# Kernel tuning notes

Hardware: AMD Instinct MI355X
Metric: run time of the kernel (lower is better)

## Reference

```python
import jax, jax.numpy as jnp
import numpy as np
from jax import lax

GAIN = 16.0           # encoder_gains[0]
TEMP = 0.3            # soft_round_temperature
MASK = 9              # mask_size
PAD = 4               # (MASK - 1) // 2
# dim_arm = 16 causal taps inside the 9x9 mask (all indices < center index 40)
CTX_IDX = [12, 13, 14, 20, 21, 22, 23, 24, 28, 29, 30, 31, 32, 33, 38, 39]
CTX_OFF = [(i // MASK, i % MASK) for i in CTX_IDX]
IMG_H, IMG_W = 1024, 1536
N_GRIDS = 7
SIZES = [(int(np.ceil(IMG_H / 2 ** i)), int(np.ceil(IMG_W / 2 ** i))) for i in range(N_GRIDS)]
N_TOTAL = sum(h * w for h, w in SIZES)  # 2097024


def _softround(x, t):
    fl = jnp.floor(x)
    return fl + 0.5 * jnp.tanh((x - fl - 0.5) / t) / jnp.tanh(0.5 / t) + 0.5


def _forward(latents, noise_u, arm_w1, arm_b1, arm_w2, arm_b2, arm_wo, arm_bo,
             ups_k, pre_k, syn_w1, syn_b1, syn_w2, syn_b2):
    # --- quantize latents: softround(softround(x*g) + kumaraswamy noise), a=1 -> uniform-0.5 ---
    flat = jnp.concatenate([l.reshape(-1) for l in latents]) * GAIN
    flat_q = _softround(_softround(flat, TEMP) + (noise_u - 0.5), TEMP)
    dec, cnt = [], 0
    for h, w in SIZES:
        dec.append(flat_q[cnt:cnt + h * w].reshape(1, 1, h, w))
        cnt += h * w
    # --- _get_neighbor: masked causal context gather (16 taps of the 9x9 mask) ---
    ctxs = []
    for l in dec:
        h, w = l.shape[2], l.shape[3]
        xp = jnp.pad(l[0, 0], PAD)  # zero pad, matches F.pad constant 0
        ctxs.append(jnp.stack([xp[dy:dy + h, dx:dx + w] for dy, dx in CTX_OFF], axis=-1).reshape(-1, len(CTX_OFF)))
    ctx = jnp.concatenate(ctxs, axis=0)  # [N, 16]
    # --- ARM MLP: residual hidden layers, final linear to (mu, log_scale) ---
    h1 = jax.nn.relu(ctx @ arm_w1.T + arm_b1 + ctx)
    h2 = jax.nn.relu(h1 @ arm_w2.T + arm_b2 + h1)
    raw = h2 @ arm_wo.T + arm_bo
    mu, log_s = raw[:, 0], raw[:, 1]
    scale = jnp.exp(-0.5 * jnp.clip(log_s, -13.8155, 13.8155))
    def lcdf(x):
        return 0.5 - 0.5 * jnp.sign(x - mu) * jnp.expm1(-jnp.abs(x - mu) / scale)
    proba = jnp.maximum(lcdf(flat_q + 0.5) - lcdf(flat_q - 0.5), 2.0 ** -16)
    rate = -jnp.log2(proba)
    # --- upsampling: coarse-to-fine, depthwise separable convT x2 + preconcat filter ---
    x = dec[-1]
    for step, i in enumerate(range(N_GRIDS - 1, 0, -1)):
        c = x.shape[1]
        kern = jnp.broadcast_to(jnp.outer(ups_k[step], ups_k[step])[None, None], (c, 1, 8, 8))
        x = lax.conv_general_dilated(x, kern, (1, 1), ((4, 4), (4, 4)), lhs_dilation=(2, 2),
                                     dimension_numbers=('NCHW', 'OIHW', 'NCHW'), feature_group_count=c)
        ht, wt = SIZES[i - 1]
        x = x[:, :, :ht, :wt]
        pk2 = jnp.outer(pre_k[step], pre_k[step])[None, None]  # (1,1,7,7)
        t = lax.conv_general_dilated(dec[i - 1], pk2, (1, 1), ((3, 3), (3, 3)),
                                     dimension_numbers=('NCHW', 'OIHW', 'NCHW'))
        x = jnp.concatenate([t, x], axis=1)
    # --- synthesis: 1x1 conv 7->48 relu, 48->6, split mean / log_scale ---
    hid = jax.nn.relu(jnp.einsum('bchw,oc->bohw', x, syn_w1) + syn_b1[None, :, None, None])
    out = jnp.einsum('bchw,oc->bohw', hid, syn_w2) + syn_b2[None, :, None, None]
    pixel_mean, pixel_log_scale = out[:, :3], out[:, 3:]
    # F.interpolate to img_size is identity here (already full resolution)
    decoded = jnp.clip(pixel_mean, 0.0, 1.0)
    return pixel_mean, pixel_log_scale, decoded, rate


def setup_inputs():
    key = jax.random.key(0)
    ks = jax.random.split(key, 16)
    d = {}
    for i, (h, w) in enumerate(SIZES):
        d['latent%d' % i] = jax.random.uniform(ks[i], (1, 1, h, w), jnp.float32, -0.5, 0.5)
    d['noise_u'] = jax.random.uniform(ks[7], (N_TOTAL,), jnp.float32)
    d['arm_w1'] = jax.random.normal(ks[8], (16, 16), jnp.float32) * 0.25
    d['arm_b1'] = jnp.zeros((16,), jnp.float32)
    d['arm_w2'] = jax.random.normal(ks[9], (16, 16), jnp.float32) * 0.25
    d['arm_b2'] = jnp.zeros((16,), jnp.float32)
    d['arm_wo'] = jax.random.normal(ks[10], (2, 16), jnp.float32) * 0.25
    d['arm_bo'] = jnp.zeros((2,), jnp.float32)
    d['ups_k'] = jax.random.normal(ks[11], (6, 8), jnp.float32) * 0.2 + 0.125
    d['pre_k'] = jax.random.normal(ks[12], (6, 7), jnp.float32) * 0.2 + 0.1
    d['syn_w1'] = jax.random.normal(ks[13], (48, 7), jnp.float32) * 0.3
    d['syn_b1'] = jnp.zeros((48,), jnp.float32)
    d['syn_w2'] = jax.random.normal(ks[14], (6, 48), jnp.float32) * 0.1
    d['syn_b2'] = jnp.zeros((6,), jnp.float32)
    return d


def reference(latent0, latent1, latent2, latent3, latent4, latent5, latent6, noise_u,
              arm_w1, arm_b1, arm_w2, arm_b2, arm_wo, arm_bo,
              ups_k, pre_k, syn_w1, syn_b1, syn_w2, syn_b2):
    return _forward([latent0, latent1, latent2, latent3, latent4, latent5, latent6], noise_u,
                    arm_w1, arm_b1, arm_w2, arm_b2, arm_wo, arm_bo,
                    ups_k, pre_k, syn_w1, syn_b1, syn_w2, syn_b2)
```

## Files before the change

kernel.cpp:

```cpp
#include <hip/hip_runtime.h>
#include <math.h>

#define N_TOTAL 2097024
#define HWF (1024 * 1536)

#define OFF0 0
#define OFF1 1572864
#define OFF2 1966080
#define OFF3 2064384
#define OFF4 2088960
#define OFF5 2095104
#define OFF6 2096640

#define OUT_LS   (3 * HWF)
#define OUT_DEC  (6 * HWF)
#define OUT_RATE (9 * HWF)

typedef float f4 __attribute__((ext_vector_type(4), aligned(4)));

__device__ __forceinline__ float softround_f(float x) {
    const float INV_T = 1.0f / 0.3f;
    const float HALF_OVER_TANH = 0.53699381f;
    float fl = floorf(x);
    return fl + tanhf((x - fl - 0.5f) * INV_T) * HALF_OVER_TANH + 0.5f;
}

__global__ void quant_kernel(const float* __restrict__ l0, const float* __restrict__ l1,
                             const float* __restrict__ l2, const float* __restrict__ l3,
                             const float* __restrict__ l4, const float* __restrict__ l5,
                             const float* __restrict__ l6, const float* __restrict__ noise,
                             float* __restrict__ flat_q) {
    int idx = blockIdx.x * blockDim.x + threadIdx.x;
    if (idx >= N_TOTAL) return;
    float v;
    if      (idx < OFF1) v = l0[idx - OFF0];
    else if (idx < OFF2) v = l1[idx - OFF1];
    else if (idx < OFF3) v = l2[idx - OFF2];
    else if (idx < OFF4) v = l3[idx - OFF3];
    else if (idx < OFF5) v = l4[idx - OFF4];
    else if (idx < OFF6) v = l5[idx - OFF5];
    else                 v = l6[idx - OFF6];
    float x = v * 16.0f;
    float s1 = softround_f(x);
    float s2 = softround_f(s1 + noise[idx] - 0.5f);
    flat_q[idx] = s2;
}

template <int H, int W, int OFFT>
__device__ __forceinline__ void arm_body(const float* __restrict__ flat_q, int pos,
                                         const float* __restrict__ w1, const float* __restrict__ b1,
                                         const float* __restrict__ w2, const float* __restrict__ b2,
                                         const float* __restrict__ wo, const float* __restrict__ bo,
                                         float* __restrict__ rate_out) {
    if (pos >= H * W) return;
    unsigned up = (unsigned)pos;
    int y = up / (unsigned)W;
    int x = pos - y * W;
    const float* g = flat_q + OFFT;

    const int DY[16] = {-3,-3,-3,-2,-2,-2,-2,-2,-1,-1,-1,-1,-1,-1, 0, 0};
    const int DX[16] = {-1, 0, 1,-2,-1, 0, 1, 2,-3,-2,-1, 0, 1, 2,-2,-1};
    float ctx[16];
#pragma unroll
    for (int k = 0; k < 16; k++) {
        int yy = y + DY[k], xx = x + DX[k];
        ctx[k] = (yy >= 0 && yy < H && xx >= 0 && xx < W) ? g[yy * W + xx] : 0.0f;
    }

    float h1[16];
#pragma unroll 4
    for (int j = 0; j < 16; j++) {
        float acc = b1[j] + ctx[j];
#pragma unroll
        for (int k = 0; k < 16; k++) acc = fmaf(w1[j * 16 + k], ctx[k], acc);
        h1[j] = fmaxf(acc, 0.0f);
    }
    float h2[16];
#pragma unroll 4
    for (int j = 0; j < 16; j++) {
        float acc = b2[j] + h1[j];
#pragma unroll
        for (int k = 0; k < 16; k++) acc = fmaf(w2[j * 16 + k], h1[k], acc);
        h2[j] = fmaxf(acc, 0.0f);
    }
    float mu = bo[0], ls = bo[1];
#pragma unroll
    for (int k = 0; k < 16; k++) {
        mu = fmaf(wo[k], h2[k], mu);
        ls = fmaf(wo[16 + k], h2[k], ls);
    }
    ls = fminf(fmaxf(ls, -13.8155f), 13.8155f);
    float inv_scale = expf(0.5f * ls);

    float q = g[(size_t)y * W + x];
    float da = (q + 0.5f) - mu;
    float db = (q - 0.5f) - mu;
    float la = 0.5f - 0.5f * copysignf(1.0f, da) * expm1f(-fabsf(da) * inv_scale);
    float lb = 0.5f - 0.5f * copysignf(1.0f, db) * expm1f(-fabsf(db) * inv_scale);
    float proba = fmaxf(la - lb, 1.52587890625e-05f);
    rate_out[OFFT + pos] = -log2f(proba);
}

__global__ __launch_bounds__(256) void arm_all_kernel(
    const float* __restrict__ flat_q,
    const float* __restrict__ w1, const float* __restrict__ b1,
    const float* __restrict__ w2, const float* __restrict__ b2,
    const float* __restrict__ wo, const float* __restrict__ bo,
    float* __restrict__ rate_out) {
    int b = blockIdx.x;
    int t = threadIdx.x;
    if (b < 6144) {
        arm_body<1024, 1536, OFF0>(flat_q, b * 256 + t, w1, b1, w2, b2, wo, bo, rate_out);
    } else if (b < 7680) {
        arm_body<512, 768, OFF1>(flat_q, (b - 6144) * 256 + t, w1, b1, w2, b2, wo, bo, rate_out);
    } else if (b < 8064) {
        arm_body<256, 384, OFF2>(flat_q, (b - 7680) * 256 + t, w1, b1, w2, b2, wo, bo, rate_out);
    } else if (b < 8160) {
        arm_body<128, 192, OFF3>(flat_q, (b - 8064) * 256 + t, w1, b1, w2, b2, wo, bo, rate_out);
    } else if (b < 8184) {
        arm_body<64, 96, OFF4>(flat_q, (b - 8160) * 256 + t, w1, b1, w2, b2, wo, bo, rate_out);
    } else if (b < 8190) {
        arm_body<32, 48, OFF5>(flat_q, (b - 8184) * 256 + t, w1, b1, w2, b2, wo, bo, rate_out);
    } else {
        arm_body<16, 24, OFF6>(flat_q, (b - 8190) * 256 + t, w1, b1, w2, b2, wo, bo, rate_out);
    }
}

__device__ __forceinline__ void up_quad(const float* __restrict__ in, int H, int W,
                                        int i, int j, const float* K, float o[4]) {
    float w[5][5];
    bool interior = (i >= 2 && i <= H - 3 && j >= 2 && j <= W - 3);
    if (interior) {
        const float* p = in + (i - 2) * W + (j - 2);
#pragma unroll
        for (int r = 0; r < 5; r++) {
            f4 a = *(const f4*)p;
            w[r][0] = a.x; w[r][1] = a.y; w[r][2] = a.z; w[r][3] = a.w;
            w[r][4] = p[4];
            p += W;
        }
    } else {
#pragma unroll
        for (int r = 0; r < 5; r++)
#pragma unroll
            for (int e = 0; e < 5; e++) {
                int yy = i - 2 + r, xx = j - 2 + e;
                w[r][e] = (yy >= 0 && yy < H && xx >= 0 && xx < W) ? in[yy * W + xx] : 0.0f;
            }
    }
    float h0[5], h1[5];
#pragma unroll
    for (int r = 0; r < 5; r++) {
        h0[r] = K[0]*w[r][0] + K[2]*w[r][1] + K[4]*w[r][2] + K[6]*w[r][3];
        h1[r] = K[1]*w[r][1] + K[3]*w[r][2] + K[5]*w[r][3] + K[7]*w[r][4];
    }
    o[0] = K[0]*h0[0] + K[2]*h0[1] + K[4]*h0[2] + K[6]*h0[3];
    o[1] = K[0]*h1[0] + K[2]*h1[1] + K[4]*h1[2] + K[6]*h1[3];
    o[2] = K[1]*h0[1] + K[3]*h0[2] + K[5]*h0[3] + K[7]*h0[4];
    o[3] = K[1]*h1[1] + K[3]*h1[2] + K[5]*h1[3] + K[7]*h1[4];
}

__device__ __forceinline__ void conv7_quad(const float* __restrict__ dec, int H, int W,
                                           int i, int j, const float* k, float o[4]) {
    int Y = 2 * i, X = 2 * j;
    float g0[8], g1[8];
    bool interior = (Y - 3 >= 0 && Y + 4 <= H - 1 && X - 3 >= 0 && X + 4 <= W - 1);
    if (interior) {
        const float* p = dec + (Y - 3) * W + (X - 3);
#pragma unroll
        for (int r = 0; r < 8; r++) {
            f4 a = *(const f4*)p;
            f4 b = *(const f4*)(p + 4);
            g0[r] = k[0]*a.x + k[1]*a.y + k[2]*a.z + k[3]*a.w + k[4]*b.x + k[5]*b.y + k[6]*b.z;
            g1[r] = k[0]*a.y + k[1]*a.z + k[2]*a.w + k[3]*b.x + k[4]*b.y + k[5]*b.z + k[6]*b.w;
            p += W;
        }
    } else {
#pragma unroll
        for (int r = 0; r < 8; r++) {
            float wv[8];
#pragma unroll
            for (int q = 0; q < 8; q++) {
                int yy = Y - 3 + r, xx = X - 3 + q;
                wv[q] = (yy >= 0 && yy < H && xx >= 0 && xx < W) ? dec[yy * W + xx] : 0.0f;
            }
            g0[r] = k[0]*wv[0] + k[1]*wv[1] + k[2]*wv[2] + k[3]*wv[3] + k[4]*wv[4] + k[5]*wv[5] + k[6]*wv[6];
            g1[r] = k[0]*wv[1] + k[1]*wv[2] + k[2]*wv[3] + k[3]*wv[4] + k[4]*wv[5] + k[5]*wv[6] + k[6]*wv[7];
        }
    }
    o[0] = k[0]*g0[0] + k[1]*g0[1] + k[2]*g0[2] + k[3]*g0[3] + k[4]*g0[4] + k[5]*g0[5] + k[6]*g0[6];
    o[1] = k[0]*g1[0] + k[1]*g1[1] + k[2]*g1[2] + k[3]*g1[3] + k[4]*g1[4] + k[5]*g1[5] + k[6]*g1[6];
    o[2] = k[0]*g0[1] + k[1]*g0[2] + k[2]*g0[3] + k[3]*g0[4] + k[4]*g0[5] + k[5]*g0[6] + k[6]*g0[7];
    o[3] = k[0]*g1[1] + k[1]*g1[2] + k[2]*g1[3] + k[3]*g1[4] + k[4]*g1[5] + k[5]*g1[6] + k[6]*g1[7];
}

__global__ void pyramid_quad_kernel(const float* __restrict__ xin, int hin, int win_,
                                    const float* __restrict__ dec,
                                    const float* __restrict__ upsk, const float* __restrict__ prek,
                                    float* __restrict__ xout, int hout, int wout) {
    int qw = wout >> 1, qh = hout >> 1;
    int j = blockIdx.x * blockDim.x + threadIdx.x;
    int i = blockIdx.y * blockDim.y + threadIdx.y;
    int c = blockIdx.z;
    if (j >= qw || i >= qh) return;
    float o[4];
    if (c == 0) {
        float k[7];
#pragma unroll
        for (int p = 0; p < 7; p++) k[p] = prek[p];
        conv7_quad(dec, hout, wout, i, j, k, o);
    } else {
        float K[8];
#pragma unroll
        for (int p = 0; p < 8; p++) K[p] = upsk[p];
        up_quad(xin + (size_t)(c - 1) * hin * win_, hin, win_, i, j, K, o);
    }
    size_t base = ((size_t)c * hout + 2 * i) * wout + 2 * j;
    *(float2*)(xout + base)        = make_float2(o[0], o[1]);
    *(float2*)(xout + base + wout) = make_float2(o[2], o[3]);
}

__global__ __launch_bounds__(256) void final_kernel(
    const float* __restrict__ up_in,
    const float* __restrict__ dec0,
    const float* __restrict__ upsk, const float* __restrict__ prek,
    const float* __restrict__ w1, const float* __restrict__ b1,
    const float* __restrict__ w2, const float* __restrict__ b2,
    float* __restrict__ out) {
    const int H2_ = 512, W2_ = 768, H1_ = 1024, W1_ = 1536;
    int t = threadIdx.x;
    int j = blockIdx.x * 16 + (t & 15);
    int i = blockIdx.y * 16 + (t >> 4);

    float K[8], kp[7];
#pragma unroll
    for (int p = 0; p < 8; p++) K[p] = upsk[p];
#pragma unroll
    for (int p = 0; p < 7; p++) kp[p] = prek[p];

    float px0[7], px1[7], px2[7], px3[7];
    {
        float o[4];
        conv7_quad(dec0, H1_, W1_, i, j, kp, o);
        px0[0] = o[0]; px1[0] = o[1]; px2[0] = o[2]; px3[0] = o[3];
    }
#pragma unroll
    for (int c = 0; c < 6; c++) {
        float o[4];
        up_quad(up_in + (size_t)c * (H2_ * W2_), H2_, W2_, i, j, K, o);
        px0[c + 1] = o[0]; px1[c + 1] = o[1]; px2[c + 1] = o[2]; px3[c + 1] = o[3];
    }

    float o0[6], o1[6], o2[6], o3[6];
#pragma unroll
    for (int q = 0; q < 6; q++) {
        float bq = b2[q];
        o0[q] = bq; o1[q] = bq; o2[q] = bq; o3[q] = bq;
    }
#pragma unroll 4
    for (int k = 0; k < 48; k++) {
        float bk = b1[k];
        float a0 = bk, a1 = bk, a2 = bk, a3 = bk;
#pragma unroll
        for (int c = 0; c < 7; c++) {
            float wk = w1[k * 7 + c];
            a0 = fmaf(wk, px0[c], a0);
            a1 = fmaf(wk, px1[c], a1);
            a2 = fmaf(wk, px2[c], a2);
            a3 = fmaf(wk, px3[c], a3);
        }
        a0 = fmaxf(a0, 0.0f); a1 = fmaxf(a1, 0.0f); a2 = fmaxf(a2, 0.0f); a3 = fmaxf(a3, 0.0f);
#pragma unroll
        for (int q = 0; q < 6; q++) {
            float wj = w2[q * 48 + k];
            o0[q] = fmaf(wj, a0, o0[q]);
            o1[q] = fmaf(wj, a1, o1[q]);
            o2[q] = fmaf(wj, a2, o2[q]);
            o3[q] = fmaf(wj, a3, o3[q]);
        }
    }

    size_t base = (size_t)(2 * i) * W1_ + 2 * j;
#pragma unroll
    for (int c = 0; c < 3; c++) {
        *(float2*)(out + (size_t)c * HWF + base)       = make_float2(o0[c], o1[c]);
        *(float2*)(out + (size_t)c * HWF + base + W1_) = make_float2(o2[c], o3[c]);
        *(float2*)(out + OUT_LS + (size_t)c * HWF + base)       = make_float2(o0[c + 3], o1[c + 3]);
        *(float2*)(out + OUT_LS + (size_t)c * HWF + base + W1_) = make_float2(o2[c + 3], o3[c + 3]);
        *(float2*)(out + OUT_DEC + (size_t)c * HWF + base) =
            make_float2(fminf(fmaxf(o0[c], 0.0f), 1.0f), fminf(fmaxf(o1[c], 0.0f), 1.0f));
        *(float2*)(out + OUT_DEC + (size_t)c * HWF + base + W1_) =
            make_float2(fminf(fmaxf(o2[c], 0.0f), 1.0f), fminf(fmaxf(o3[c], 0.0f), 1.0f));
    }
}

extern "C" void kernel_launch(void* const* d_in, const int* in_sizes, int n_in,
                              void* d_out, int out_size, void* d_ws, size_t ws_size,
                              hipStream_t stream) {
    const float* lat[7];
    for (int i = 0; i < 7; i++) lat[i] = (const float*)d_in[i];
    const float* noise  = (const float*)d_in[7];
    const float* arm_w1 = (const float*)d_in[8];
    const float* arm_b1 = (const float*)d_in[9];
    const float* arm_w2 = (const float*)d_in[10];
    const float* arm_b2 = (const float*)d_in[11];
    const float* arm_wo = (const float*)d_in[12];
    const float* arm_bo = (const float*)d_in[13];
    const float* ups_k  = (const float*)d_in[14];
    const float* pre_k  = (const float*)d_in[15];
    const float* syn_w1 = (const float*)d_in[16];
    const float* syn_b1 = (const float*)d_in[17];
    const float* syn_w2 = (const float*)d_in[18];
    const float* syn_b2 = (const float*)d_in[19];
    float* out = (float*)d_out;

    float* flat_q = (float*)d_ws;
    float* bufA   = flat_q + N_TOTAL;
    float* bufB   = bufA + 6 * 512 * 768;

    static const int SH[7]  = {1024, 512, 256, 128, 64, 32, 16};
    static const int SW[7]  = {1536, 768, 384, 192, 96, 48, 24};
    static const int OFF[7] = {OFF0, OFF1, OFF2, OFF3, OFF4, OFF5, OFF6};

    quant_kernel<<<(N_TOTAL + 255) / 256, 256, 0, stream>>>(
        lat[0], lat[1], lat[2], lat[3], lat[4], lat[5], lat[6], noise, flat_q);

    arm_all_kernel<<<8192, 256, 0, stream>>>(flat_q, arm_w1, arm_b1, arm_w2, arm_b2,
                                             arm_wo, arm_bo, out + OUT_RATE);

    const float* xin = flat_q + OFF6;
    float* bufs[2] = {bufA, bufB};
    for (int s = 0; s < 5; s++) {
        int i    = 6 - s;
        int hin  = SH[i], win_ = SW[i];
        int hout = SH[i - 1], wout = SW[i - 1];
        int cin  = s + 1;
        float* xout = bufs[s & 1];
        dim3 blk(16, 16);
        dim3 grd((wout / 2 + 15) / 16, (hout / 2 + 15) / 16, cin + 1);
        pyramid_quad_kernel<<<grd, blk, 0, stream>>>(xin, hin, win_,
                                                     flat_q + OFF[i - 1],
                                                     ups_k + s * 8, pre_k + s * 7,
                                                     xout, hout, wout);
        xin = xout;
    }

    dim3 fgrd(768 / 16, 512 / 16);
    final_kernel<<<fgrd, 256, 0, stream>>>(bufA, flat_q,
                                           ups_k + 5 * 8, pre_k + 5 * 7,
                                           syn_w1, syn_b1, syn_w2, syn_b2, out);
}
```

Baseline: 149.6 us.

## Use packed fp16 dot2 for synthesis MLP and fast tanh in softround

```diff
diff --git a/kernel.cpp b/kernel.cpp
--- a/kernel.cpp
+++ b/kernel.cpp
@@ -17,12 +17,52 @@
 #define OUT_RATE (9 * HWF)
 
 typedef float f4 __attribute__((ext_vector_type(4), aligned(4)));
+typedef _Float16 h2 __attribute__((ext_vector_type(2)));
+typedef __fp16 fp16v2 __attribute__((ext_vector_type(2)));
+
+__device__ __forceinline__ h2 as_h2(unsigned u) {
+    union { unsigned u; h2 h; } x; x.u = u; return x.h;
+}
+__device__ __forceinline__ h2 pkrtz(float a, float b) {
+    union { fp16v2 f; h2 h; } x;
+    x.f = __builtin_amdgcn_cvt_pkrtz(a, b);
+    return x.h;
+}
+__device__ __forceinline__ float dot2f(h2 a, h2 b, float c) {
+#if __has_builtin(__builtin_amdgcn_fdot2)
+    return __builtin_amdgcn_fdot2(a, b, c, false);
+#else
+    return fmaf((float)a[0], (float)b[0], fmaf((float)a[1], (float)b[1], c));
+#endif
+}
 
 __device__ __forceinline__ float softround_f(float x) {
     const float INV_T = 1.0f / 0.3f;
     const float HALF_OVER_TANH = 0.53699381f;
     float fl = floorf(x);
-    return fl + tanhf((x - fl - 0.5f) * INV_T) * HALF_OVER_TANH + 0.5f;
+    float z = (x - fl - 0.5f) * INV_T;
+    float e = __expf(2.0f * z);
+    float th = 1.0f - 2.0f * __builtin_amdgcn_rcpf(e + 1.0f);
+    return fl + th * HALF_OVER_TANH + 0.5f;
+}
+
+__global__ void pack_weights_kernel(const float* __restrict__ w1, const float* __restrict__ b1,
+                                    const float* __restrict__ w2, unsigned* __restrict__ wp) {
+    int t = threadIdx.x;
+    if (t < 192) {
+        int k = t >> 2, p = t & 3;
+        float x = w1[k * 7 + 2 * p];
+        float y = (p < 3) ? w1[k * 7 + 2 * p + 1] : b1[k];
+        union { h2 h; unsigned u; } c;
+        c.h = (h2){(_Float16)x, (_Float16)y};
+        wp[t] = c.u;
+    } else if (t < 336) {
+        int r = t - 192;
+        int o = r / 24, kk = r - o * 24;
+        union { h2 h; unsigned u; } c;
+        c.h = (h2){(_Float16)w2[o * 48 + 2 * kk], (_Float16)w2[o * 48 + 2 * kk + 1]};
+        wp[t] = c.u;
+    }
 }
 
 __global__ void quant_kernel(const float* __restrict__ l0, const float* __restrict__ l1,
@@ -75,19 +115,19 @@
         for (int k = 0; k < 16; k++) acc = fmaf(w1[j * 16 + k], ctx[k], acc);
         h1[j] = fmaxf(acc, 0.0f);
     }
-    float h2[16];
+    float h2v[16];
 #pragma unroll 4
     for (int j = 0; j < 16; j++) {
         float acc = b2[j] + h1[j];
 #pragma unroll
         for (int k = 0; k < 16; k++) acc = fmaf(w2[j * 16 + k], h1[k], acc);
-        h2[j] = fmaxf(acc, 0.0f);
+        h2v[j] = fmaxf(acc, 0.0f);
     }
     float mu = bo[0], ls = bo[1];
 #pragma unroll
     for (int k = 0; k < 16; k++) {
-        mu = fmaf(wo[k], h2[k], mu);
-        ls = fmaf(wo[16 + k], h2[k], ls);
+        mu = fmaf(wo[k], h2v[k], mu);
+        ls = fmaf(wo[16 + k], h2v[k], ls);
     }
     ls = fminf(fmaxf(ls, -13.8155f), 13.8155f);
     float inv_scale = expf(0.5f * ls);
@@ -224,8 +264,8 @@
     const float* __restrict__ up_in,
     const float* __restrict__ dec0,
     const float* __restrict__ upsk, const float* __restrict__ prek,
-    const float* __restrict__ w1, const float* __restrict__ b1,
-    const float* __restrict__ w2, const float* __restrict__ b2,
+    const unsigned* __restrict__ wp,
+    const float* __restrict__ b2,
     float* __restrict__ out) {
     const int H2_ = 512, W2_ = 768, H1_ = 1024, W1_ = 1536;
     int t = threadIdx.x;
@@ -251,46 +291,72 @@
         px0[c + 1] = o[0]; px1[c + 1] = o[1]; px2[c + 1] = o[2]; px3[c + 1] = o[3];
     }
 
-    float o0[6], o1[6], o2[6], o3[6];
-#pragma unroll
-    for (int q = 0; q < 6; q++) {
-        float bq = b2[q];
-        o0[q] = bq; o1[q] = bq; o2[q] = bq; o3[q] = bq;
-    }
+    h2 pp[4][4];
+#pragma unroll
+    for (int c = 0; c < 3; c++) {
+        pp[0][c] = pkrtz(px0[2 * c], px0[2 * c + 1]);
+        pp[1][c] = pkrtz(px1[2 * c], px1[2 * c + 1]);
+        pp[2][c] = pkrtz(px2[2 * c], px2[2 * c + 1]);
+        pp[3][c] = pkrtz(px3[2 * c], px3[2 * c + 1]);
+    }
+    pp[0][3] = pkrtz(px0[6], 1.0f);
+    pp[1][3] = pkrtz(px1[6], 1.0f);
+    pp[2][3] = pkrtz(px2[6], 1.0f);
+    pp[3][3] = pkrtz(px3[6], 1.0f);
+
+    float acc[6][4];
+#pragma unroll
+    for (int o = 0; o < 6; o++) {
+        float b = b2[o];
+#pragma unroll
+        for (int q = 0; q < 4; q++) acc[o][q] = b;
+    }
+    const unsigned* w1p = wp;
+    const unsigned* w2p = wp + 192;
 #pragma unroll 4
-    for (int k = 0; k < 48; k++) {
-        float bk = b1[k];
-        float a0 = bk, a1 = bk, a2 = bk, a3 = bk;
-#pragma unroll
-        for (int c = 0; c < 7; c++) {
-            float wk = w1[k * 7 + c];
-            a0 = fmaf(wk, px0[c], a0);
-            a1 = fmaf(wk, px1[c], a1);
-            a2 = fmaf(wk, px2[c], a2);
-            a3 = fmaf(wk, px3[c], a3);
-        }
-        a0 = fmaxf(a0, 0.0f); a1 = fmaxf(a1, 0.0f); a2 = fmaxf(a2, 0.0f); a3 = fmaxf(a3, 0.0f);
-#pragma unroll
-        for (int q = 0; q < 6; q++) {
-            float wj = w2[q * 48 + k];
-            o0[q] = fmaf(wj, a0, o0[q]);
-            o1[q] = fmaf(wj, a1, o1[q]);
-            o2[q] = fmaf(wj, a2, o2[q]);
-            o3[q] = fmaf(wj, a3, o3[q]);
+    for (int kk = 0; kk < 24; kk++) {
+        h2 wk0[4], wk1[4];
+#pragma unroll
+        for (int p = 0; p < 4; p++) {
+            wk0[p] = as_h2(w1p[(2 * kk) * 4 + p]);
+            wk1[p] = as_h2(w1p[(2 * kk + 1) * 4 + p]);
+        }
+        float a0[4], a1[4];
+#pragma unroll
+        for (int q = 0; q < 4; q++) {
+            float s0 = 0.0f, s1 = 0.0f;
+#pragma unroll
+            for (int p = 0; p < 4; p++) {
+                s0 = dot2f(wk0[p], pp[q][p], s0);
+                s1 = dot2f(wk1[p], pp[q][p], s1);
+            }
+            a0[q] = fmaxf(s0, 0.0f);
+            a1[q] = fmaxf(s1, 0.0f);
+        }
+        h2 hp[4];
+#pragma unroll
+        for (int q = 0; q < 4; q++)
+            hp[q] = pkrtz(a0[q], a1[q]);
+#pragma unroll
+        for (int o = 0; o < 6; o++) {
+            h2 w2k = as_h2(w2p[o * 24 + kk]);
+#pragma unroll
+            for (int q = 0; q < 4; q++)
+                acc[o][q] = dot2f(w2k, hp[q], acc[o][q]);
         }
     }
 
     size_t base = (size_t)(2 * i) * W1_ + 2 * j;
 #pragma unroll
     for (int c = 0; c < 3; c++) {
-        *(float2*)(out + (size_t)c * HWF + base)       = make_float2(o0[c], o1[c]);
-        *(float2*)(out + (size_t)c * HWF + base + W1_) = make_float2(o2[c], o3[c]);
-        *(float2*)(out + OUT_LS + (size_t)c * HWF + base)       = make_float2(o0[c + 3], o1[c + 3]);
-        *(float2*)(out + OUT_LS + (size_t)c * HWF + base + W1_) = make_float2(o2[c + 3], o3[c + 3]);
+        *(float2*)(out + (size_t)c * HWF + base)       = make_float2(acc[c][0], acc[c][1]);
+        *(float2*)(out + (size_t)c * HWF + base + W1_) = make_float2(acc[c][2], acc[c][3]);
+        *(float2*)(out + OUT_LS + (size_t)c * HWF + base)       = make_float2(acc[c + 3][0], acc[c + 3][1]);
+        *(float2*)(out + OUT_LS + (size_t)c * HWF + base + W1_) = make_float2(acc[c + 3][2], acc[c + 3][3]);
         *(float2*)(out + OUT_DEC + (size_t)c * HWF + base) =
-            make_float2(fminf(fmaxf(o0[c], 0.0f), 1.0f), fminf(fmaxf(o1[c], 0.0f), 1.0f));
+            make_float2(fminf(fmaxf(acc[c][0], 0.0f), 1.0f), fminf(fmaxf(acc[c][1], 0.0f), 1.0f));
         *(float2*)(out + OUT_DEC + (size_t)c * HWF + base + W1_) =
-            make_float2(fminf(fmaxf(o2[c], 0.0f), 1.0f), fminf(fmaxf(o3[c], 0.0f), 1.0f));
+            make_float2(fminf(fmaxf(acc[c][2], 0.0f), 1.0f), fminf(fmaxf(acc[c][3], 0.0f), 1.0f));
     }
 }
 
@@ -317,10 +383,13 @@
     float* flat_q = (float*)d_ws;
     float* bufA   = flat_q + N_TOTAL;
     float* bufB   = bufA + 6 * 512 * 768;
+    unsigned* wpack = (unsigned*)(bufB + 5 * 256 * 384);
 
     static const int SH[7]  = {1024, 512, 256, 128, 64, 32, 16};
     static const int SW[7]  = {1536, 768, 384, 192, 96, 48, 24};
     static const int OFF[7] = {OFF0, OFF1, OFF2, OFF3, OFF4, OFF5, OFF6};
+
+    pack_weights_kernel<<<1, 512, 0, stream>>>(syn_w1, syn_b1, syn_w2, wpack);
 
     quant_kernel<<<(N_TOTAL + 255) / 256, 256, 0, stream>>>(
         lat[0], lat[1], lat[2], lat[3], lat[4], lat[5], lat[6], noise, flat_q);
@@ -334,10 +403,9 @@
         int i    = 6 - s;
         int hin  = SH[i], win_ = SW[i];
         int hout = SH[i - 1], wout = SW[i - 1];
-        int cin  = s + 1;
         float* xout = bufs[s & 1];
         dim3 blk(16, 16);
-        dim3 grd((wout / 2 + 15) / 16, (hout / 2 + 15) / 16, cin + 1);
+        dim3 grd((wout / 2 + 15) / 16, (hout / 2 + 15) / 16, s + 2);
         pyramid_quad_kernel<<<grd, blk, 0, stream>>>(xin, hin, win_,
                                                      flat_q + OFF[i - 1],
                                                      ups_k + s * 8, pre_k + s * 7,
@@ -348,5 +416,5 @@
     dim3 fgrd(768 / 16, 512 / 16);
     final_kernel<<<fgrd, 256, 0, stream>>>(bufA, flat_q,
                                            ups_k + 5 * 8, pre_k + 5 * 7,
-                                           syn_w1, syn_b1, syn_w2, syn_b2, out);
-}
+                                           wpack, syn_b2, out);
+}
```

After: 148.6 us. No clear change (-0.6%).
